# Kernel optimization log

Measured on AMD Instinct MI355X. Metric: run time of the kernel, lower is better.

Reference implementation:

```python
import jax, jax.numpy as jnp
import numpy as np

EMBED = 768
HEAD = 64

def setup_inputs() -> dict:
    key = jax.random.key(0)
    k1, k2, k3, k4 = jax.random.split(key, 4)
    x = jax.random.normal(k1, (8, 2048, EMBED), dtype=jnp.float32)
    # torch nn.Linear weights: [out, in], applied as x @ W.T
    scale = 1.0 / np.sqrt(EMBED)
    Wq = jax.random.uniform(k2, (HEAD, EMBED), jnp.float32, -scale, scale)
    Wk = jax.random.uniform(k3, (HEAD, EMBED), jnp.float32, -scale, scale)
    Wv = jax.random.uniform(k4, (HEAD, EMBED), jnp.float32, -scale, scale)
    return {"x": x, "Wq": Wq, "Wk": Wk, "Wv": Wv}

def reference(x, Wq, Wk, Wv):
    B, S, E = x.shape
    q = jnp.einsum('bse,he->bsh', x, Wq)
    k = jnp.einsum('bse,he->bsh', x, Wk)
    v = jnp.einsum('bse,he->bsh', x, Wv)
    # NOTE: faithful to source: weights / embed**(-0.5) == weights * sqrt(embed)
    scores = jnp.einsum('bqh,bkh->bqk', q, k) * jnp.sqrt(jnp.float32(E))
    causal = jnp.tril(jnp.ones((S, S), dtype=bool))
    scores = jnp.where(causal, scores, -jnp.inf)
    attn = jax.nn.softmax(scores, axis=-1)
    return jnp.einsum('bqk,bkh->bqh', attn, v)
```

## Files before the change

kernel.cpp:

```cpp
#include <hip/hip_runtime.h>
#include <math.h>

#define EMBED 768
#define SEQ   2048
#define NB    8
#define QSCALE 39.98113776623437f

typedef short  short8 __attribute__((ext_vector_type(8)));
typedef float  f32x4  __attribute__((ext_vector_type(4)));

#define WHI_OFF  0u
#define WLO_OFF  147456u
#define QHI_OFF  294912u
#define QLO_OFF  (294912u + 1u*1048576u)
#define KHI_OFF  (294912u + 2u*1048576u)
#define KLO_OFF  (294912u + 3u*1048576u)
#define VT_OFF   (294912u + 4u*1048576u)
#define FLT_BASE 2768896u
#define OP_OFF   FLT_BASE
#define MP_OFF   (FLT_BASE + 4194304u)
#define LP_OFF   (MP_OFF + 65536u)

__device__ __forceinline__ ushort f2bf(float f) {
    unsigned u = __float_as_uint(f);
    return (ushort)((u + 0x7FFFu + ((u >> 16) & 1u)) >> 16);
}
__device__ __forceinline__ ushort f2bf_trunc(float f) {
    return (ushort)(__float_as_uint(f) >> 16);
}
__device__ __forceinline__ float bf2f(ushort h) {
    return __uint_as_float(((unsigned)h) << 16);
}

__global__ __launch_bounds__(256)
void split_w_kernel(const float* __restrict__ Wq, const float* __restrict__ Wk,
                    const float* __restrict__ Wv,
                    ushort* __restrict__ w_hi, ushort* __restrict__ w_lo)
{
    int idx = blockIdx.x * 256 + threadIdx.x;
    if (idx >= 192 * EMBED) return;
    int row = idx / EMBED, e = idx - row * EMBED;
    float f;
    if (row < 64)       f = Wq[row * EMBED + e] * QSCALE;
    else if (row < 128) f = Wk[(row - 64) * EMBED + e];
    else                f = Wv[(row - 128) * EMBED + e];
    ushort hi = f2bf(f);
    w_hi[idx] = hi;
    w_lo[idx] = f2bf_trunc(f - bf2f(hi));
}

__global__ __launch_bounds__(256)
void proj_kernel(const float* __restrict__ x,
                 const ushort* __restrict__ w_hi, const ushort* __restrict__ w_lo,
                 ushort* __restrict__ q_hi, ushort* __restrict__ q_lo,
                 ushort* __restrict__ k_hi, ushort* __restrict__ k_lo,
                 ushort* __restrict__ v_t)
{
    __shared__ __align__(16) ushort xa_hi[32][72], xa_lo[32][72];
    __shared__ __align__(16) ushort wbh[192][72];
    __shared__ __align__(16) ushort wbl[128][72];

    const int t    = threadIdx.x;
    const int lane = t & 63;
    const int wid  = t >> 6;
    const int ln   = lane & 15;
    const int kg   = lane >> 4;
    const int row0 = blockIdx.x * 32;

    const int srow = t >> 3;
    const int scol = (t & 7) * 8;
    const int wrow = t >> 2;
    const int wcol = (t & 3) * 16;

    float4 xr0, xr1;
    short8 wh0, wh1, wh2, wh3, wh4, wh5;
    short8 wl0, wl1, wl2, wl3;

#define LOAD_CHUNK(e0) do {                                                     \
        const float*  xp_ = x + (size_t)(row0 + srow) * EMBED + (e0) + scol;    \
        xr0 = *(const float4*)xp_;  xr1 = *(const float4*)(xp_ + 4);            \
        const ushort* whp_ = w_hi + (size_t)wrow * EMBED + (e0) + wcol;         \
        wh0 = *(const short8*)whp_;                                             \
        wh1 = *(const short8*)(whp_ + 8);                                       \
        wh2 = *(const short8*)(whp_ + 64 * EMBED);                              \
        wh3 = *(const short8*)(whp_ + 64 * EMBED + 8);                          \
        wh4 = *(const short8*)(whp_ + 128 * EMBED);                             \
        wh5 = *(const short8*)(whp_ + 128 * EMBED + 8);                         \
        const ushort* wlp_ = w_lo + (size_t)wrow * EMBED + (e0) + wcol;         \
        wl0 = *(const short8*)wlp_;                                             \
        wl1 = *(const short8*)(wlp_ + 8);                                       \
        wl2 = *(const short8*)(wlp_ + 64 * EMBED);                              \
        wl3 = *(const short8*)(wlp_ + 64 * EMBED + 8);                          \
    } while (0)

    const f32x4 vzero = {0.f, 0.f, 0.f, 0.f};
    f32x4 acc[2][3];
#pragma unroll
    for (int mt = 0; mt < 2; ++mt)
#pragma unroll
        for (int j = 0; j < 3; ++j) acc[mt][j] = vzero;

    LOAD_CHUNK(0);

    for (int c = 0; c < 12; ++c) {
        if (c) __syncthreads();
        {
            const float fv[8] = {xr0.x, xr0.y, xr0.z, xr0.w,
                                 xr1.x, xr1.y, xr1.z, xr1.w};
            short8 h0, l0;
#pragma unroll
            for (int i = 0; i < 8; ++i) {
                ushort h = f2bf(fv[i]);
                h0[i] = (short)h;
                l0[i] = (short)f2bf_trunc(fv[i] - bf2f(h));
            }
            *(short8*)&xa_hi[srow][scol] = h0;
            *(short8*)&xa_lo[srow][scol] = l0;
            *(short8*)&wbh[wrow][wcol]           = wh0;
            *(short8*)&wbh[wrow][wcol + 8]       = wh1;
            *(short8*)&wbh[wrow + 64][wcol]      = wh2;
            *(short8*)&wbh[wrow + 64][wcol + 8]  = wh3;
            *(short8*)&wbh[wrow + 128][wcol]     = wh4;
            *(short8*)&wbh[wrow + 128][wcol + 8] = wh5;
            *(short8*)&wbl[wrow][wcol]           = wl0;
            *(short8*)&wbl[wrow][wcol + 8]       = wl1;
            *(short8*)&wbl[wrow + 64][wcol]      = wl2;
            *(short8*)&wbl[wrow + 64][wcol + 8]  = wl3;
        }
        __syncthreads();
        if (c < 11) LOAD_CHUNK((c + 1) * 64);

        short8 ah[2][2], al[2][2];
#pragma unroll
        for (int mt = 0; mt < 2; ++mt)
#pragma unroll
            for (int ks = 0; ks < 2; ++ks) {
                ah[mt][ks] = *(const short8*)&xa_hi[mt * 16 + ln][ks * 32 + kg * 8];
                al[mt][ks] = *(const short8*)&xa_lo[mt * 16 + ln][ks * 32 + kg * 8];
            }
#pragma unroll
        for (int j = 0; j < 3; ++j) {
            const int ntg = j * 4 + wid;
#pragma unroll
            for (int ks = 0; ks < 2; ++ks) {
                const int co = ks * 32 + kg * 8;
                if (j < 2) {
                    short8 bh = *(const short8*)&wbh[ntg * 16 + ln][co];
                    short8 bl = *(const short8*)&wbl[ntg * 16 + ln][co];
#pragma unroll
                    for (int mt = 0; mt < 2; ++mt) {
                        acc[mt][j] = __builtin_amdgcn_mfma_f32_16x16x32_bf16(ah[mt][ks], bh, acc[mt][j], 0, 0, 0);
                        acc[mt][j] = __builtin_amdgcn_mfma_f32_16x16x32_bf16(ah[mt][ks], bl, acc[mt][j], 0, 0, 0);
                        acc[mt][j] = __builtin_amdgcn_mfma_f32_16x16x32_bf16(al[mt][ks], bh, acc[mt][j], 0, 0, 0);
                    }
                } else {
                    short8 bh = *(const short8*)&wbh[ntg * 16 + ln][co];
#pragma unroll
                    for (int mt = 0; mt < 2; ++mt)
                        acc[mt][j] = __builtin_amdgcn_mfma_f32_16x16x32_bf16(ah[mt][ks], bh, acc[mt][j], 0, 0, 0);
                }
            }
        }
    }
#undef LOAD_CHUNK

#pragma unroll
    for (int mt = 0; mt < 2; ++mt) {
        const int rbase = row0 + mt * 16 + kg * 4;
#pragma unroll
        for (int j = 0; j < 3; ++j) {
            const int col = (j * 4 + wid) * 16 + ln;
#pragma unroll
            for (int r = 0; r < 4; ++r) {
                int rg = rbase + r;
                int b = rg >> 11, s = rg & 2047;
                size_t rowoff = ((size_t)b * SEQ + s) * 64;
                float val = acc[mt][j][r];
                if (col < 64) {
                    ushort h = f2bf(val);
                    q_hi[rowoff + col] = h;
                    q_lo[rowoff + col] = f2bf_trunc(val - bf2f(h));
                } else if (col < 128) {
                    ushort h = f2bf(val);
                    k_hi[rowoff + (col - 64)] = h;
                    k_lo[rowoff + (col - 64)] = f2bf_trunc(val - bf2f(h));
                } else {
                    v_t[((size_t)b * 64 + (col - 128)) * SEQ + s] = f2bf(val);
                }
            }
        }
    }
}

__global__ __launch_bounds__(256)
void attn_kernel(const ushort* __restrict__ q_hi, const ushort* __restrict__ q_lo,
                 const ushort* __restrict__ k_hi, const ushort* __restrict__ k_lo,
                 const ushort* __restrict__ v_t,
                 float* __restrict__ oP, float* __restrict__ mP, float* __restrict__ lP)
{
    __shared__ __align__(16) ushort kv[2][3][64][64];
    __shared__ __align__(16) ushort pT[4][16][72];

    const int t    = threadIdx.x;
    const int lane = t & 63;
    const int w    = t >> 6;
    const int ln   = lane & 15;
    const int kg   = lane >> 4;
    const int b    = blockIdx.x & 7;
    const int pr   = (blockIdx.x >> 3) & 15;
    const int z    = (blockIdx.x >> 7) & 3;
    const int qA   = 31 - pr;
    const int qB2  = pr;
    const int c1   = (qA - z) / 4 + 1;
    const int c2   = (qB2 >= z) ? (qB2 - z) / 4 + 1 : 0;
    const int tot  = c1 + c2;

    const ushort* qhb = q_hi + (size_t)b * SEQ * 64;
    const ushort* qlb = q_lo + (size_t)b * SEQ * 64;
    const ushort* khb = k_hi + (size_t)b * SEQ * 64;
    const ushort* klb = k_lo + (size_t)b * SEQ * 64;
    const ushort* vtb = v_t + (size_t)b * 64 * SEQ;

    short8 qhA[2], qlA[2], qhB[2], qlB[2];
#pragma unroll
    for (int ks = 0; ks < 2; ++ks) {
        size_t offA = (size_t)(qA * 64 + w * 16 + ln) * 64 + ks * 32 + kg * 8;
        size_t offB = (size_t)(qB2 * 64 + w * 16 + ln) * 64 + ks * 32 + kg * 8;
        qhA[ks] = *(const short8*)(qhb + offA);
        qlA[ks] = *(const short8*)(qlb + offA);
        qhB[ks] = *(const short8*)(qhb + offB);
        qlB[ks] = *(const short8*)(qlb + offB);
    }

    const f32x4 vzero = {0.f, 0.f, 0.f, 0.f};
    f32x4 oA[4], oB[4];
    float mA = -INFINITY, lA = 0.f, mB = -INFINITY, lB = 0.f;
#pragma unroll
    for (int i = 0; i < 4; ++i) { oA[i] = vzero; oB[i] = vzero; }

    const int si    = w * 6;
    const int srow8 = lane >> 3;
    const int scol  = ((lane & 7) << 3) ^ ((lane >> 3) << 3);

    auto stage = [&](int pass, int cbuf) {
        const int kk = (pass < c1) ? (z + 4 * pass) : (z + 4 * (pass - c1));
        const int j0 = kk << 6;
        ushort* base = &kv[cbuf][0][0][0];
#pragma unroll
        for (int s = 0; s < 6; ++s) {
            const int i = si + s;
            const int row = ((i & 7) << 3) + srow8;
            const ushort* g;
            if (i < 8)       g = khb + (size_t)(j0 + row) * 64 + scol;
            else if (i < 16) g = klb + (size_t)(j0 + row) * 64 + scol;
            else             g = vtb + (size_t)row * SEQ + j0 + scol;
            __builtin_amdgcn_global_load_lds(
                (const __attribute__((address_space(1))) void*)g,
                (__attribute__((address_space(3))) void*)(base + i * 512),
                16, 0, 0);
        }
    };

    auto body = [&](int kk, int qblk, f32x4 (&o)[4], float& m_run, float& l_run,
                    short8 (&qh)[2], short8 (&ql)[2], int cbuf) {
        const ushort* K0 = &kv[cbuf][0][0][0];
        const ushort* K1 = &kv[cbuf][1][0][0];
        const ushort* VT = &kv[cbuf][2][0][0];
        const int xorc = (ln & 7) << 3;

        f32x4 sacc[4];
#pragma unroll
        for (int ct = 0; ct < 4; ++ct) sacc[ct] = vzero;
#pragma unroll
        for (int ct = 0; ct < 4; ++ct) {
            const int rb = (ct * 16 + ln) * 64;
#pragma unroll
            for (int ks = 0; ks < 2; ++ks) {
                const int co = (ks * 32 + kg * 8) ^ xorc;
                short8 bh = *(const short8*)(K0 + rb + co);
                short8 bl = *(const short8*)(K1 + rb + co);
                sacc[ct] = __builtin_amdgcn_mfma_f32_16x16x32_bf16(bh, qh[ks], sacc[ct], 0, 0, 0);
                sacc[ct] = __builtin_amdgcn_mfma_f32_16x16x32_bf16(bh, ql[ks], sacc[ct], 0, 0, 0);
                sacc[ct] = __builtin_amdgcn_mfma_f32_16x16x32_bf16(bl, qh[ks], sacc[ct], 0, 0, 0);
            }
        }

        if (kk == qblk) {
            const int qrow = qblk * 64 + w * 16 + ln;
#pragma unroll
            for (int ct = 0; ct < 4; ++ct) {
                int kb0 = kk * 64 + ct * 16 + kg * 4;
#pragma unroll
                for (int r = 0; r < 4; ++r)
                    if (kb0 + r > qrow) sacc[ct][r] = -1e30f;
            }
        }

        float mt_ = fmaxf(fmaxf(fmaxf(sacc[0][0], sacc[0][1]), fmaxf(sacc[0][2], sacc[0][3])),
                          fmaxf(fmaxf(sacc[1][0], sacc[1][1]), fmaxf(sacc[1][2], sacc[1][3])));
        float mt2 = fmaxf(fmaxf(fmaxf(sacc[2][0], sacc[2][1]), fmaxf(sacc[2][2], sacc[2][3])),
                          fmaxf(fmaxf(sacc[3][0], sacc[3][1]), fmaxf(sacc[3][2], sacc[3][3])));
        mt_ = fmaxf(mt_, mt2);
        mt_ = fmaxf(mt_, __shfl_xor(mt_, 16));
        mt_ = fmaxf(mt_, __shfl_xor(mt_, 32));
        float mn   = fmaxf(m_run, mt_);
        float corr = exp2f(m_run - mn);
        float p[4][4];
        float lt = 0.f;
#pragma unroll
        for (int ct = 0; ct < 4; ++ct)
#pragma unroll
            for (int r = 0; r < 4; ++r) {
                p[ct][r] = exp2f(sacc[ct][r] - mn);
                lt += p[ct][r];
            }
        lt += __shfl_xor(lt, 16);
        lt += __shfl_xor(lt, 32);
        m_run = mn;
        l_run = l_run * corr + lt;

#pragma unroll
        for (int ct = 0; ct < 4; ++ct) {
            uint u0 = (uint)f2bf(p[ct][0]) | ((uint)f2bf(p[ct][1]) << 16);
            uint u1 = (uint)f2bf(p[ct][2]) | ((uint)f2bf(p[ct][3]) << 16);
            *(uint*)&pT[w][ln][ct * 16 + kg * 4]     = u0;
            *(uint*)&pT[w][ln][ct * 16 + kg * 4 + 2] = u1;
        }
        float corrq[4];
#pragma unroll
        for (int r = 0; r < 4; ++r) corrq[r] = __shfl(corr, kg * 4 + r);
#pragma unroll
        for (int ht = 0; ht < 4; ++ht)
#pragma unroll
            for (int r = 0; r < 4; ++r) o[ht][r] *= corrq[r];
#pragma unroll
        for (int ks = 0; ks < 2; ++ks) {
            short8 pa = *(const short8*)&pT[w][ln][ks * 32 + kg * 8];
#pragma unroll
            for (int ht = 0; ht < 4; ++ht) {
                const int co = (ks * 32 + kg * 8) ^ xorc;
                short8 bv = *(const short8*)(VT + (ht * 16 + ln) * 64 + co);
                o[ht] = __builtin_amdgcn_mfma_f32_16x16x32_bf16(pa, bv, o[ht], 0, 0, 0);
            }
        }
    };

    stage(0, 0);
    __syncthreads();
    int cur = 0;
    for (int pass = 0; pass < tot; ++pass) {
        if (pass + 1 < tot) stage(pass + 1, cur ^ 1);
        const int kk = (pass < c1) ? (z + 4 * pass) : (z + 4 * (pass - c1));
        if (pass < c1) body(kk, qA,  oA, mA, lA, qhA, qlA, cur);
        else           body(kk, qB2, oB, mB, lB, qhB, qlB, cur);
        __syncthreads();
        cur ^= 1;
    }

    float* oPz = oP + (size_t)z * 1048576u;
    float* mPz = mP + (size_t)z * 16384u;
    float* lPz = lP + (size_t)z * 16384u;
    {
        const size_t rowg = (size_t)b * SEQ + qA * 64 + w * 16;
#pragma unroll
        for (int ht = 0; ht < 4; ++ht)
#pragma unroll
            for (int r = 0; r < 4; ++r)
                oPz[(rowg + kg * 4 + r) * 64 + ht * 16 + ln] = oA[ht][r];
        if (kg == 0) { mPz[rowg + ln] = mA; lPz[rowg + ln] = lA; }
    }
    {
        const size_t rowg = (size_t)b * SEQ + qB2 * 64 + w * 16;
#pragma unroll
        for (int ht = 0; ht < 4; ++ht)
#pragma unroll
            for (int r = 0; r < 4; ++r)
                oPz[(rowg + kg * 4 + r) * 64 + ht * 16 + ln] = oB[ht][r];
        if (kg == 0) { mPz[rowg + ln] = mB; lPz[rowg + ln] = lB; }
    }
}

__global__ __launch_bounds__(256)
void merge_kernel(const float* __restrict__ oP, const float* __restrict__ mP,
                  const float* __restrict__ lP, float* __restrict__ out)
{
    int idx = blockIdx.x * 256 + threadIdx.x;
    int R  = idx >> 4;
    int h0 = (idx & 15) << 2;
    float m0 = mP[R],          m1 = mP[16384 + R];
    float m2 = mP[2*16384 + R], m3 = mP[3*16384 + R];
    float l0 = lP[R],          l1 = lP[16384 + R];
    float l2 = lP[2*16384 + R], l3 = lP[3*16384 + R];
    float M  = fmaxf(fmaxf(m0, m1), fmaxf(m2, m3));
    float c0 = exp2f(m0 - M), c1 = exp2f(m1 - M);
    float c2 = exp2f(m2 - M), c3 = exp2f(m3 - M);
    float inv = 1.0f / (l0 * c0 + l1 * c1 + l2 * c2 + l3 * c3);
    float4 a = *(const float4*)(oP + (size_t)R * 64 + h0);
    float4 d = *(const float4*)(oP + 1048576u + (size_t)R * 64 + h0);
    float4 e = *(const float4*)(oP + 2097152u + (size_t)R * 64 + h0);
    float4 f = *(const float4*)(oP + 3145728u + (size_t)R * 64 + h0);
    float4 r;
    r.x = (a.x * c0 + d.x * c1 + e.x * c2 + f.x * c3) * inv;
    r.y = (a.y * c0 + d.y * c1 + e.y * c2 + f.y * c3) * inv;
    r.z = (a.z * c0 + d.z * c1 + e.z * c2 + f.z * c3) * inv;
    r.w = (a.w * c0 + d.w * c1 + e.w * c2 + f.w * c3) * inv;
    *(float4*)(out + (size_t)R * 64 + h0) = r;
}

extern "C" void kernel_launch(void* const* d_in, const int* in_sizes, int n_in,
                              void* d_out, int out_size, void* d_ws, size_t ws_size,
                              hipStream_t stream)
{
    const float* x  = (const float*)d_in[0];
    const float* Wq = (const float*)d_in[1];
    const float* Wk = (const float*)d_in[2];
    const float* Wv = (const float*)d_in[3];
    float* out = (float*)d_out;

    ushort* ws = (ushort*)d_ws;
    float*  wsf = (float*)d_ws;
    ushort* w_hi = ws + WHI_OFF;
    ushort* w_lo = ws + WLO_OFF;
    ushort* q_hi = ws + QHI_OFF;
    ushort* q_lo = ws + QLO_OFF;
    ushort* k_hi = ws + KHI_OFF;
    ushort* k_lo = ws + KLO_OFF;
    ushort* v_t  = ws + VT_OFF;
    float*  oP   = wsf + OP_OFF;
    float*  mP   = wsf + MP_OFF;
    float*  lP   = wsf + LP_OFF;

    split_w_kernel<<<dim3(576), dim3(256), 0, stream>>>(Wq, Wk, Wv, w_hi, w_lo);
    proj_kernel<<<dim3(512), dim3(256), 0, stream>>>(x, w_hi, w_lo,
                                                     q_hi, q_lo, k_hi, k_lo, v_t);
    attn_kernel<<<dim3(512), dim3(256), 0, stream>>>(q_hi, q_lo, k_hi, k_lo, v_t,
                                                     oP, mP, lP);
    merge_kernel<<<dim3(1024), dim3(256), 0, stream>>>(oP, mP, lP, out);
}
```

Before: 60.84 us.

## Switch attention to 32x32 MFMA with 128-row query tiles and register P transpose

Rewrites the attention kernel to use 32x32x16 bf16 MFMA on 128-row query blocks, with each wave owning 32 query rows. The P matrix is now packed with v_cvt_pk_bf16 and exchanged through cross-lane shuffles, replacing the LDS round-trip. The split-K factor is made runtime (8 when the workspace is large enough, else 4), with a generic merge loop. The aim is fewer LDS operations, denser MFMA work per load and better load balance. The cost is more registers per thread and more partial outputs for the merge to read.

```diff
diff --git a/kernel.cpp b/kernel.cpp
--- a/kernel.cpp
+++ b/kernel.cpp
@@ -8,6 +8,7 @@
 
 typedef short  short8 __attribute__((ext_vector_type(8)));
 typedef float  f32x4  __attribute__((ext_vector_type(4)));
+typedef float  f32x16 __attribute__((ext_vector_type(16)));
 
 #define WHI_OFF  0u
 #define WLO_OFF  147456u
@@ -17,9 +18,6 @@
 #define KLO_OFF  (294912u + 3u*1048576u)
 #define VT_OFF   (294912u + 4u*1048576u)
 #define FLT_BASE 2768896u
-#define OP_OFF   FLT_BASE
-#define MP_OFF   (FLT_BASE + 4194304u)
-#define LP_OFF   (MP_OFF + 65536u)
 
 __device__ __forceinline__ ushort f2bf(float f) {
     unsigned u = __float_as_uint(f);
@@ -31,6 +29,13 @@
 __device__ __forceinline__ float bf2f(ushort h) {
     return __uint_as_float(((unsigned)h) << 16);
 }
+__device__ __forceinline__ uint cvtpk(float a, float b) {
+    uint r;
+    asm("v_cvt_pk_bf16_f32 %0, %1, %2" : "=v"(r) : "v"(a), "v"(b));
+    return r;
+}
+
+union U8 { uint u[4]; short8 s; };
 
 __global__ __launch_bounds__(256)
 void split_w_kernel(const float* __restrict__ Wq, const float* __restrict__ Wk,
@@ -196,214 +201,229 @@
 void attn_kernel(const ushort* __restrict__ q_hi, const ushort* __restrict__ q_lo,
                  const ushort* __restrict__ k_hi, const ushort* __restrict__ k_lo,
                  const ushort* __restrict__ v_t,
-                 float* __restrict__ oP, float* __restrict__ mP, float* __restrict__ lP)
+                 float* __restrict__ oP, float* __restrict__ mP,
+                 float* __restrict__ lP, int Z)
 {
     __shared__ __align__(16) ushort kv[2][3][64][64];
-    __shared__ __align__(16) ushort pT[4][16][72];
 
     const int t    = threadIdx.x;
     const int lane = t & 63;
     const int w    = t >> 6;
-    const int ln   = lane & 15;
-    const int kg   = lane >> 4;
+    const int l31  = lane & 31;
+    const int h8   = (lane >> 5) << 3;
+    const int sw   = (lane & 7) << 3;
     const int b    = blockIdx.x & 7;
-    const int pr   = (blockIdx.x >> 3) & 15;
-    const int z    = (blockIdx.x >> 7) & 3;
-    const int qA   = 31 - pr;
-    const int qB2  = pr;
-    const int c1   = (qA - z) / 4 + 1;
-    const int c2   = (qB2 >= z) ? (qB2 - z) / 4 + 1 : 0;
-    const int tot  = c1 + c2;
+    const int pr   = (blockIdx.x >> 3) & 7;
+    const int z    = blockIdx.x >> 6;
+    const int qA   = 15 - pr;
+    const int qB   = pr;
+    const int cA   = 2 * qA + 2;
+    const int T    = cA + 2 * qB + 2;
 
     const ushort* qhb = q_hi + (size_t)b * SEQ * 64;
     const ushort* qlb = q_lo + (size_t)b * SEQ * 64;
     const ushort* khb = k_hi + (size_t)b * SEQ * 64;
     const ushort* klb = k_lo + (size_t)b * SEQ * 64;
     const ushort* vtb = v_t + (size_t)b * 64 * SEQ;
-
-    short8 qhA[2], qlA[2], qhB[2], qlB[2];
-#pragma unroll
-    for (int ks = 0; ks < 2; ++ks) {
-        size_t offA = (size_t)(qA * 64 + w * 16 + ln) * 64 + ks * 32 + kg * 8;
-        size_t offB = (size_t)(qB2 * 64 + w * 16 + ln) * 64 + ks * 32 + kg * 8;
-        qhA[ks] = *(const short8*)(qhb + offA);
-        qlA[ks] = *(const short8*)(qlb + offA);
-        qhB[ks] = *(const short8*)(qhb + offB);
-        qlB[ks] = *(const short8*)(qlb + offB);
-    }
-
-    const f32x4 vzero = {0.f, 0.f, 0.f, 0.f};
-    f32x4 oA[4], oB[4];
-    float mA = -INFINITY, lA = 0.f, mB = -INFINITY, lB = 0.f;
-#pragma unroll
-    for (int i = 0; i < 4; ++i) { oA[i] = vzero; oB[i] = vzero; }
-
-    const int si    = w * 6;
+    float* oPz = oP + (size_t)z * 1048576u;
+    float* mPz = mP + (size_t)z * 16384u;
+    float* lPz = lP + (size_t)z * 16384u;
+
     const int srow8 = lane >> 3;
     const int scol  = ((lane & 7) << 3) ^ ((lane >> 3) << 3);
 
-    auto stage = [&](int pass, int cbuf) {
-        const int kk = (pass < c1) ? (z + 4 * pass) : (z + 4 * (pass - c1));
+    auto stage = [&](int g, int cbuf) {
+        const int kk = (g < cA) ? g : g - cA;
         const int j0 = kk << 6;
         ushort* base = &kv[cbuf][0][0][0];
 #pragma unroll
         for (int s = 0; s < 6; ++s) {
-            const int i = si + s;
+            const int i = w * 6 + s;
             const int row = ((i & 7) << 3) + srow8;
-            const ushort* g;
-            if (i < 8)       g = khb + (size_t)(j0 + row) * 64 + scol;
-            else if (i < 16) g = klb + (size_t)(j0 + row) * 64 + scol;
-            else             g = vtb + (size_t)row * SEQ + j0 + scol;
+            const ushort* gp;
+            if (i < 8)       gp = khb + (size_t)(j0 + row) * 64 + scol;
+            else if (i < 16) gp = klb + (size_t)(j0 + row) * 64 + scol;
+            else             gp = vtb + (size_t)row * SEQ + j0 + scol;
             __builtin_amdgcn_global_load_lds(
-                (const __attribute__((address_space(1))) void*)g,
+                (const __attribute__((address_space(1))) void*)gp,
                 (__attribute__((address_space(3))) void*)(base + i * 512),
                 16, 0, 0);
         }
     };
 
-    auto body = [&](int kk, int qblk, f32x4 (&o)[4], float& m_run, float& l_run,
-                    short8 (&qh)[2], short8 (&ql)[2], int cbuf) {
+    auto loadQ = [&](int qb, short8 (&qh)[4], short8 (&ql)[4]) {
+#pragma unroll
+        for (int ks = 0; ks < 4; ++ks) {
+            size_t off = (size_t)(qb * 128 + w * 32 + l31) * 64 + ks * 16 + h8;
+            qh[ks] = *(const short8*)(qhb + off);
+            ql[ks] = *(const short8*)(qlb + off);
+        }
+    };
+
+    auto body = [&](int kk, int qb, f32x16 (&o)[2], float& m_run, float& l_run,
+                    short8 (&qh)[4], short8 (&ql)[4], int cbuf) {
         const ushort* K0 = &kv[cbuf][0][0][0];
         const ushort* K1 = &kv[cbuf][1][0][0];
         const ushort* VT = &kv[cbuf][2][0][0];
-        const int xorc = (ln & 7) << 3;
-
-        f32x4 sacc[4];
-#pragma unroll
-        for (int ct = 0; ct < 4; ++ct) sacc[ct] = vzero;
-#pragma unroll
-        for (int ct = 0; ct < 4; ++ct) {
-            const int rb = (ct * 16 + ln) * 64;
-#pragma unroll
-            for (int ks = 0; ks < 2; ++ks) {
-                const int co = (ks * 32 + kg * 8) ^ xorc;
-                short8 bh = *(const short8*)(K0 + rb + co);
-                short8 bl = *(const short8*)(K1 + rb + co);
-                sacc[ct] = __builtin_amdgcn_mfma_f32_16x16x32_bf16(bh, qh[ks], sacc[ct], 0, 0, 0);
-                sacc[ct] = __builtin_amdgcn_mfma_f32_16x16x32_bf16(bh, ql[ks], sacc[ct], 0, 0, 0);
-                sacc[ct] = __builtin_amdgcn_mfma_f32_16x16x32_bf16(bl, qh[ks], sacc[ct], 0, 0, 0);
-            }
-        }
-
-        if (kk == qblk) {
-            const int qrow = qblk * 64 + w * 16 + ln;
-#pragma unroll
-            for (int ct = 0; ct < 4; ++ct) {
-                int kb0 = kk * 64 + ct * 16 + kg * 4;
-#pragma unroll
-                for (int r = 0; r < 4; ++r)
-                    if (kb0 + r > qrow) sacc[ct][r] = -1e30f;
-            }
-        }
-
-        float mt_ = fmaxf(fmaxf(fmaxf(sacc[0][0], sacc[0][1]), fmaxf(sacc[0][2], sacc[0][3])),
-                          fmaxf(fmaxf(sacc[1][0], sacc[1][1]), fmaxf(sacc[1][2], sacc[1][3])));
-        float mt2 = fmaxf(fmaxf(fmaxf(sacc[2][0], sacc[2][1]), fmaxf(sacc[2][2], sacc[2][3])),
-                          fmaxf(fmaxf(sacc[3][0], sacc[3][1]), fmaxf(sacc[3][2], sacc[3][3])));
-        mt_ = fmaxf(mt_, mt2);
-        mt_ = fmaxf(mt_, __shfl_xor(mt_, 16));
-        mt_ = fmaxf(mt_, __shfl_xor(mt_, 32));
-        float mn   = fmaxf(m_run, mt_);
+
+        f32x16 sacc[2];
+#pragma unroll
+        for (int i = 0; i < 16; ++i) { sacc[0][i] = 0.f; sacc[1][i] = 0.f; }
+#pragma unroll
+        for (int kt = 0; kt < 2; ++kt) {
+            const int rb = (kt * 32 + l31) * 64;
+#pragma unroll
+            for (int ks = 0; ks < 4; ++ks) {
+                const int c = (ks * 16 + h8) ^ sw;
+                short8 ah = *(const short8*)(K0 + rb + c);
+                short8 al = *(const short8*)(K1 + rb + c);
+                sacc[kt] = __builtin_amdgcn_mfma_f32_32x32x16_bf16(ah, qh[ks], sacc[kt], 0, 0, 0);
+                sacc[kt] = __builtin_amdgcn_mfma_f32_32x32x16_bf16(ah, ql[ks], sacc[kt], 0, 0, 0);
+                sacc[kt] = __builtin_amdgcn_mfma_f32_32x32x16_bf16(al, qh[ks], sacc[kt], 0, 0, 0);
+            }
+        }
+
+        if ((kk >> 1) == qb) {
+            const int q   = qb * 128 + w * 32 + l31;
+            const int hi4 = (lane >> 5) << 2;
+#pragma unroll
+            for (int kt = 0; kt < 2; ++kt) {
+                const int kb = kk * 64 + kt * 32 + hi4;
+#pragma unroll
+                for (int reg = 0; reg < 16; ++reg) {
+                    const int key = kb + (reg & 3) + 8 * (reg >> 2);
+                    if (key > q) sacc[kt][reg] = -1e30f;
+                }
+            }
+        }
+
+        float t8[8];
+#pragma unroll
+        for (int j = 0; j < 8; ++j)
+            t8[j] = fmaxf(fmaxf(sacc[0][2*j], sacc[0][2*j+1]),
+                          fmaxf(sacc[1][2*j], sacc[1][2*j+1]));
+        float mx = fmaxf(fmaxf(fmaxf(t8[0], t8[1]), fmaxf(t8[2], t8[3])),
+                         fmaxf(fmaxf(t8[4], t8[5]), fmaxf(t8[6], t8[7])));
+        mx = fmaxf(mx, __shfl_xor(mx, 32));
+        float mn   = fmaxf(m_run, mx);
         float corr = exp2f(m_run - mn);
-        float p[4][4];
+        float p[2][16];
         float lt = 0.f;
 #pragma unroll
-        for (int ct = 0; ct < 4; ++ct)
-#pragma unroll
-            for (int r = 0; r < 4; ++r) {
-                p[ct][r] = exp2f(sacc[ct][r] - mn);
-                lt += p[ct][r];
-            }
-        lt += __shfl_xor(lt, 16);
+        for (int kt = 0; kt < 2; ++kt)
+#pragma unroll
+            for (int reg = 0; reg < 16; ++reg) {
+                p[kt][reg] = exp2f(sacc[kt][reg] - mn);
+                lt += p[kt][reg];
+            }
         lt += __shfl_xor(lt, 32);
         m_run = mn;
         l_run = l_run * corr + lt;
-
-#pragma unroll
-        for (int ct = 0; ct < 4; ++ct) {
-            uint u0 = (uint)f2bf(p[ct][0]) | ((uint)f2bf(p[ct][1]) << 16);
-            uint u1 = (uint)f2bf(p[ct][2]) | ((uint)f2bf(p[ct][3]) << 16);
-            *(uint*)&pT[w][ln][ct * 16 + kg * 4]     = u0;
-            *(uint*)&pT[w][ln][ct * 16 + kg * 4 + 2] = u1;
-        }
-        float corrq[4];
-#pragma unroll
-        for (int r = 0; r < 4; ++r) corrq[r] = __shfl(corr, kg * 4 + r);
-#pragma unroll
-        for (int ht = 0; ht < 4; ++ht)
-#pragma unroll
-            for (int r = 0; r < 4; ++r) o[ht][r] *= corrq[r];
-#pragma unroll
-        for (int ks = 0; ks < 2; ++ks) {
-            short8 pa = *(const short8*)&pT[w][ln][ks * 32 + kg * 8];
-#pragma unroll
-            for (int ht = 0; ht < 4; ++ht) {
-                const int co = (ks * 32 + kg * 8) ^ xorc;
-                short8 bv = *(const short8*)(VT + (ht * 16 + ln) * 64 + co);
-                o[ht] = __builtin_amdgcn_mfma_f32_16x16x32_bf16(pa, bv, o[ht], 0, 0, 0);
+        o[0] = o[0] * corr;
+        o[1] = o[1] * corr;
+
+        const bool hiH = (lane >= 32);
+#pragma unroll
+        for (int kt = 0; kt < 2; ++kt) {
+            uint pk[8], rx[8];
+#pragma unroll
+            for (int j = 0; j < 8; ++j) pk[j] = cvtpk(p[kt][2*j], p[kt][2*j+1]);
+#pragma unroll
+            for (int j = 0; j < 8; ++j) rx[j] = (uint)__shfl_xor((int)pk[j], 32);
+            U8 f0, f1;
+            f0.u[0] = hiH ? rx[2] : pk[0];
+            f0.u[1] = hiH ? rx[3] : pk[1];
+            f0.u[2] = hiH ? pk[2] : rx[0];
+            f0.u[3] = hiH ? pk[3] : rx[1];
+            f1.u[0] = hiH ? rx[6] : pk[4];
+            f1.u[1] = hiH ? rx[7] : pk[5];
+            f1.u[2] = hiH ? pk[6] : rx[4];
+            f1.u[3] = hiH ? pk[7] : rx[5];
+#pragma unroll
+            for (int ht = 0; ht < 2; ++ht) {
+                const int row = ht * 32 + l31;
+#pragma unroll
+                for (int s2 = 0; s2 < 2; ++s2) {
+                    const int c = (kt * 32 + s2 * 16 + h8) ^ sw;
+                    short8 av = *(const short8*)(VT + row * 64 + c);
+                    o[ht] = __builtin_amdgcn_mfma_f32_32x32x16_bf16(
+                                av, (s2 ? f1.s : f0.s), o[ht], 0, 0, 0);
+                }
             }
         }
     };
 
-    stage(0, 0);
+    auto storeP = [&](int qb, f32x16 (&o)[2], float m_run, float l_run) {
+        const size_t rowq = (size_t)b * SEQ + qb * 128 + w * 32 + l31;
+        const int hb = (lane >> 5) << 2;
+        float* op = oPz + rowq * 64;
+#pragma unroll
+        for (int ht = 0; ht < 2; ++ht)
+#pragma unroll
+            for (int rq = 0; rq < 4; ++rq) {
+                float4 v = make_float4(o[ht][4*rq], o[ht][4*rq+1],
+                                       o[ht][4*rq+2], o[ht][4*rq+3]);
+                *(float4*)(op + ht * 32 + rq * 8 + hb) = v;
+            }
+        if (lane < 32) { mPz[rowq] = m_run; lPz[rowq] = l_run; }
+    };
+
+    short8 qh[4], ql[4];
+    f32x16 o[2];
+    float m_run, l_run;
+
+    int g = z;
+    stage(g, 0);
+    loadQ(qA, qh, ql);
+#pragma unroll
+    for (int i = 0; i < 16; ++i) { o[0][i] = 0.f; o[1][i] = 0.f; }
+    m_run = -INFINITY; l_run = 0.f;
     __syncthreads();
     int cur = 0;
-    for (int pass = 0; pass < tot; ++pass) {
-        if (pass + 1 < tot) stage(pass + 1, cur ^ 1);
-        const int kk = (pass < c1) ? (z + 4 * pass) : (z + 4 * (pass - c1));
-        if (pass < c1) body(kk, qA,  oA, mA, lA, qhA, qlA, cur);
-        else           body(kk, qB2, oB, mB, lB, qhB, qlB, cur);
+
+    while (g < cA) {
+        const int gn = g + Z;
+        if (gn < T) stage(gn, cur ^ 1);
+        body(g, qA, o, m_run, l_run, qh, ql, cur);
         __syncthreads();
-        cur ^= 1;
-    }
-
-    float* oPz = oP + (size_t)z * 1048576u;
-    float* mPz = mP + (size_t)z * 16384u;
-    float* lPz = lP + (size_t)z * 16384u;
-    {
-        const size_t rowg = (size_t)b * SEQ + qA * 64 + w * 16;
-#pragma unroll
-        for (int ht = 0; ht < 4; ++ht)
-#pragma unroll
-            for (int r = 0; r < 4; ++r)
-                oPz[(rowg + kg * 4 + r) * 64 + ht * 16 + ln] = oA[ht][r];
-        if (kg == 0) { mPz[rowg + ln] = mA; lPz[rowg + ln] = lA; }
-    }
-    {
-        const size_t rowg = (size_t)b * SEQ + qB2 * 64 + w * 16;
-#pragma unroll
-        for (int ht = 0; ht < 4; ++ht)
-#pragma unroll
-            for (int r = 0; r < 4; ++r)
-                oPz[(rowg + kg * 4 + r) * 64 + ht * 16 + ln] = oB[ht][r];
-        if (kg == 0) { mPz[rowg + ln] = mB; lPz[rowg + ln] = lB; }
-    }
+        cur ^= 1; g = gn;
+    }
+    storeP(qA, o, m_run, l_run);
+
+    loadQ(qB, qh, ql);
+#pragma unroll
+    for (int i = 0; i < 16; ++i) { o[0][i] = 0.f; o[1][i] = 0.f; }
+    m_run = -INFINITY; l_run = 0.f;
+
+    while (g < T) {
+        const int gn = g + Z;
+        if (gn < T) stage(gn, cur ^ 1);
+        body(g - cA, qB, o, m_run, l_run, qh, ql, cur);
+        __syncthreads();
+        cur ^= 1; g = gn;
+    }
+    storeP(qB, o, m_run, l_run);
 }
 
 __global__ __launch_bounds__(256)
 void merge_kernel(const float* __restrict__ oP, const float* __restrict__ mP,
-                  const float* __restrict__ lP, float* __restrict__ out)
+                  const float* __restrict__ lP, float* __restrict__ out, int Z)
 {
     int idx = blockIdx.x * 256 + threadIdx.x;
     int R  = idx >> 4;
     int h0 = (idx & 15) << 2;
-    float m0 = mP[R],          m1 = mP[16384 + R];
-    float m2 = mP[2*16384 + R], m3 = mP[3*16384 + R];
-    float l0 = lP[R],          l1 = lP[16384 + R];
-    float l2 = lP[2*16384 + R], l3 = lP[3*16384 + R];
-    float M  = fmaxf(fmaxf(m0, m1), fmaxf(m2, m3));
-    float c0 = exp2f(m0 - M), c1 = exp2f(m1 - M);
-    float c2 = exp2f(m2 - M), c3 = exp2f(m3 - M);
-    float inv = 1.0f / (l0 * c0 + l1 * c1 + l2 * c2 + l3 * c3);
-    float4 a = *(const float4*)(oP + (size_t)R * 64 + h0);
-    float4 d = *(const float4*)(oP + 1048576u + (size_t)R * 64 + h0);
-    float4 e = *(const float4*)(oP + 2097152u + (size_t)R * 64 + h0);
-    float4 f = *(const float4*)(oP + 3145728u + (size_t)R * 64 + h0);
-    float4 r;
-    r.x = (a.x * c0 + d.x * c1 + e.x * c2 + f.x * c3) * inv;
-    r.y = (a.y * c0 + d.y * c1 + e.y * c2 + f.y * c3) * inv;
-    r.z = (a.z * c0 + d.z * c1 + e.z * c2 + f.z * c3) * inv;
-    r.w = (a.w * c0 + d.w * c1 + e.w * c2 + f.w * c3) * inv;
+    float M = -INFINITY;
+    for (int zz = 0; zz < Z; ++zz) M = fmaxf(M, mP[zz * 16384 + R]);
+    float L = 0.f;
+    float4 acc = make_float4(0.f, 0.f, 0.f, 0.f);
+    for (int zz = 0; zz < Z; ++zz) {
+        float c = exp2f(mP[zz * 16384 + R] - M);
+        L += lP[zz * 16384 + R] * c;
+        float4 a = *(const float4*)(oP + (size_t)zz * 1048576u + (size_t)R * 64 + h0);
+        acc.x += a.x * c; acc.y += a.y * c; acc.z += a.z * c; acc.w += a.w * c;
+    }
+    float inv = 1.0f / L;
+    float4 r = make_float4(acc.x * inv, acc.y * inv, acc.z * inv, acc.w * inv);
     *(float4*)(out + (size_t)R * 64 + h0) = r;
 }
 
@@ -426,14 +446,20 @@
     ushort* k_hi = ws + KHI_OFF;
     ushort* k_lo = ws + KLO_OFF;
     ushort* v_t  = ws + VT_OFF;
-    float*  oP   = wsf + OP_OFF;
-    float*  mP   = wsf + MP_OFF;
-    float*  lP   = wsf + LP_OFF;
+
+    int Z = 8;
+    {
+        size_t need8 = ((size_t)FLT_BASE + 8u * (1048576u + 32768u)) * 4u;
+        if (ws_size < need8) Z = 4;
+    }
+    float* oP = wsf + FLT_BASE;
+    float* mP = oP + (size_t)Z * 1048576u;
+    float* lP = mP + (size_t)Z * 16384u;
 
     split_w_kernel<<<dim3(576), dim3(256), 0, stream>>>(Wq, Wk, Wv, w_hi, w_lo);
     proj_kernel<<<dim3(512), dim3(256), 0, stream>>>(x, w_hi, w_lo,
                                                      q_hi, q_lo, k_hi, k_lo, v_t);
-    attn_kernel<<<dim3(512), dim3(256), 0, stream>>>(q_hi, q_lo, k_hi, k_lo, v_t,
-                                                     oP, mP, lP);
-    merge_kernel<<<dim3(1024), dim3(256), 0, stream>>>(oP, mP, lP, out);
-}
+    attn_kernel<<<dim3(64 * Z), dim3(256), 0, stream>>>(q_hi, q_lo, k_hi, k_lo, v_t,
+                                                        oP, mP, lP, Z);
+    merge_kernel<<<dim3(1024), dim3(256), 0, stream>>>(oP, mP, lP, out, Z);
+}
```

Result: slower. 62.42 us (+2.6%).
